# Optimization experiments

Hardware: AMD Instinct MI355X
Metric: run time of the kernel (lower is better)

## Reference

```python
import jax, jax.numpy as jnp
import numpy as np

B, T, D = 8, 1024, 768
N_HEAD = 12
HEAD_DIM = D // N_HEAD


def setup_inputs() -> dict:
    key = jax.random.key(0)
    k1, k2, k3, k4, k5 = jax.random.split(key, 5)
    x = jax.random.normal(k1, (B, T, D), dtype=jnp.float32)
    # c_attn: Linear(D, 3D); c_proj: Linear(D, D). Stored as (in, out) for x @ W.
    s_attn = 1.0 / np.sqrt(D)
    W_attn = jax.random.uniform(k2, (D, 3 * D), dtype=jnp.float32, minval=-s_attn, maxval=s_attn)
    b_attn = jax.random.uniform(k3, (3 * D,), dtype=jnp.float32, minval=-s_attn, maxval=s_attn)
    W_proj = jax.random.uniform(k4, (D, D), dtype=jnp.float32, minval=-s_attn, maxval=s_attn)
    b_proj = jax.random.uniform(k5, (D,), dtype=jnp.float32, minval=-s_attn, maxval=s_attn)
    return {"x": x, "W_attn": W_attn, "b_attn": b_attn, "W_proj": W_proj, "b_proj": b_proj}


def reference(x, W_attn, b_attn, W_proj, b_proj):
    Bs, Ts, Ds = x.shape
    qkv = x @ W_attn + b_attn  # [B, T, 3D]
    Q, K, V = jnp.split(qkv, 3, axis=2)
    # [B, H, T, hd]
    Q = Q.reshape(Bs, Ts, N_HEAD, HEAD_DIM).transpose(0, 2, 1, 3)
    K = K.reshape(Bs, Ts, N_HEAD, HEAD_DIM).transpose(0, 2, 1, 3)
    V = V.reshape(Bs, Ts, N_HEAD, HEAD_DIM).transpose(0, 2, 1, 3)
    scale = HEAD_DIM ** (-0.5)
    scores = jnp.einsum('bhqd,bhkd->bhqk', Q, K) * scale  # [B, H, T, T]
    causal = jnp.tril(jnp.ones((Ts, Ts), dtype=bool))
    scores = jnp.where(causal[None, None, :, :], scores, -jnp.inf)
    probs = jax.nn.softmax(scores, axis=-1)
    attn = jnp.einsum('bhqk,bhkd->bhqd', probs, V)  # [B, H, T, hd]
    attn = attn.transpose(0, 2, 1, 3).reshape(Bs, Ts, Ds)
    return attn @ W_proj + b_proj
```

## Files before the change

### kernel.cpp

```cpp
#include <hip/hip_runtime.h>
#include <hip/hip_bf16.h>

#define B_ 8
#define T_ 1024
#define D_ 768
#define NH 12
#define HD 64

typedef __bf16 bf16x8 __attribute__((ext_vector_type(8)));
typedef __bf16 bf16x4 __attribute__((ext_vector_type(4)));
typedef float f32x4 __attribute__((ext_vector_type(4)));
typedef short s16x4 __attribute__((ext_vector_type(4)));

__device__ __forceinline__ float fast_exp2(float x) {
  return __builtin_amdgcn_exp2f(x);
}

__device__ __forceinline__ f32x4 mfma32(bf16x8 a, bf16x8 b, f32x4 c) {
  return __builtin_amdgcn_mfma_f32_16x16x32_bf16(a, b, c, 0, 0, 0);
}

__device__ __forceinline__ f32x4 mfma16(bf16x4 a, bf16x4 b, f32x4 c) {
  union U { bf16x4 h; s16x4 s; };
  U ua; ua.h = a;
  U ub; ub.h = b;
  return __builtin_amdgcn_mfma_f32_16x16x16bf16_1k(ua.s, ub.s, c, 0, 0, 0);
}

__device__ __forceinline__ void gload_lds16(const void* g, void* l) {
  __builtin_amdgcn_global_load_lds((const __attribute__((address_space(1))) unsigned int*)g,
                                   (__attribute__((address_space(3))) unsigned int*)l, 16, 0, 0);
}

__global__ void prep_kernel(const float* __restrict__ x, __bf16* __restrict__ xb,
                            const float* __restrict__ W_attn, __bf16* __restrict__ WaT,
                            const float* __restrict__ W_proj, __bf16* __restrict__ WpT) {
  int bid = blockIdx.x;
  int tid = threadIdx.x;
  if (bid < 3072) {
    int i = bid * 256 + tid;
    const float4* xf = (const float4*)x;
    float4 a = xf[i * 2], b = xf[i * 2 + 1];
    bf16x8 v;
    v[0] = (__bf16)a.x; v[1] = (__bf16)a.y; v[2] = (__bf16)a.z; v[3] = (__bf16)a.w;
    v[4] = (__bf16)b.x; v[5] = (__bf16)b.y; v[6] = (__bf16)b.z; v[7] = (__bf16)b.w;
    *(bf16x8*)&xb[(size_t)i * 8] = v;
    return;
  }
  __shared__ float tile[32][33];
  const float* W;
  __bf16* WT;
  int K = 768, N, n0, k0;
  if (bid < 4800) {
    int i = bid - 3072;
    W = W_attn; WT = WaT; N = 2304;
    n0 = (i % 72) * 32; k0 = (i / 72) * 32;
  } else {
    int i = bid - 4800;
    W = W_proj; WT = WpT; N = 768;
    n0 = (i % 24) * 32; k0 = (i / 24) * 32;
  }
  int col = tid & 31, r0 = tid >> 5;
#pragma unroll
  for (int p = 0; p < 4; p++) {
    int r = r0 + p * 8;
    tile[r][col] = W[(size_t)(k0 + r) * N + n0 + col];
  }
  __syncthreads();
#pragma unroll
  for (int p = 0; p < 4; p++) {
    int r = r0 + p * 8;
    WT[(size_t)(n0 + r) * K + k0 + col] = (__bf16)tile[col][r];
  }
}

__global__ __launch_bounds__(256) void gemm_qkv(const __bf16* __restrict__ A,
                                                const __bf16* __restrict__ BT,
                                                const float* __restrict__ bias,
                                                __bf16* __restrict__ Cout,
                                                __bf16* __restrict__ VT,
                                                int M, int N, int K, int nbx) {
  __shared__ __align__(16) __bf16 Asm[2][128 * 64];
  __shared__ __align__(16) __bf16 Bsm[2][64 * 64];
  int tid = threadIdx.x;
  int wave = tid >> 6, lane = tid & 63, g = lane >> 4, l15 = lane & 15;

  int wg = blockIdx.x;
  int cpx = gridDim.x >> 3;
  int wg2 = (wg & 7) * cpx + (wg >> 3);
  int bx = wg2 % nbx, by = wg2 / nbx;
  int m0 = by * 128, n0 = bx * 64;

  int srow = tid >> 3;
  int cc = (tid & 7) ^ ((tid >> 3) & 7);
  const __bf16* Ag = A + (size_t)(m0 + srow) * K + cc * 8;
  const __bf16* Bg = BT + (size_t)(n0 + srow) * K + cc * 8;

  auto stage = [&](int kt, int bf) {
#pragma unroll
    for (int i = 0; i < 4; i++)
      gload_lds16(Ag + (size_t)(i * 32) * K + kt * 64, &Asm[bf][wave * 512 + i * 2048]);
#pragma unroll
    for (int i = 0; i < 2; i++)
      gload_lds16(Bg + (size_t)(i * 32) * K + kt * 64, &Bsm[bf][wave * 512 + i * 2048]);
  };

  f32x4 zz = {0.0f, 0.0f, 0.0f, 0.0f};
  f32x4 acc[2][4];
#pragma unroll
  for (int m = 0; m < 2; m++)
#pragma unroll
    for (int n = 0; n < 4; n++) acc[m][n] = zz;

  int nk = K >> 6;
  int swr = l15 & 7;

  stage(0, 0);
  __syncthreads();

  int cur = 0;
  for (int kt = 0; kt < nk; kt++) {
    if (kt + 1 < nk) stage(kt + 1, cur ^ 1);
#pragma unroll
    for (int ks = 0; ks < 2; ks++) {
      bf16x8 af[2], bfr[4];
#pragma unroll
      for (int m = 0; m < 2; m++) {
        int row = wave * 32 + m * 16 + l15;
        af[m] = *(const bf16x8*)&Asm[cur][row * 64 + ((ks * 4 + g) ^ swr) * 8];
      }
#pragma unroll
      for (int n = 0; n < 4; n++) {
        int row = n * 16 + l15;
        bfr[n] = *(const bf16x8*)&Bsm[cur][row * 64 + ((ks * 4 + g) ^ swr) * 8];
      }
#pragma unroll
      for (int m = 0; m < 2; m++)
#pragma unroll
        for (int n = 0; n < 4; n++)
          acc[m][n] = __builtin_amdgcn_mfma_f32_16x16x32_bf16(af[m], bfr[n], acc[m][n], 0, 0, 0);
    }
    __syncthreads();
    cur ^= 1;
  }
#pragma unroll
  for (int n = 0; n < 4; n++) {
    int gcol = n0 + n * 16 + l15;
    float bv = bias[gcol];
#pragma unroll
    for (int m = 0; m < 2; m++) {
      int grow0 = m0 + wave * 32 + m * 16 + g * 4;
      float v0 = acc[m][n][0] + bv, v1 = acc[m][n][1] + bv;
      float v2 = acc[m][n][2] + bv, v3 = acc[m][n][3] + bv;
      if (gcol < 2 * D_) {
        Cout[(size_t)(grow0 + 0) * N + gcol] = (__bf16)v0;
        Cout[(size_t)(grow0 + 1) * N + gcol] = (__bf16)v1;
        Cout[(size_t)(grow0 + 2) * N + gcol] = (__bf16)v2;
        Cout[(size_t)(grow0 + 3) * N + gcol] = (__bf16)v3;
      } else {
        int hh = (gcol - 2 * D_) >> 6, dd = (gcol - 2 * D_) & 63;
        int bb = grow0 >> 10, tt = grow0 & 1023;
        bf16x4 sv = {(__bf16)v0, (__bf16)v1, (__bf16)v2, (__bf16)v3};
        *(bf16x4*)&VT[((size_t)(bb * NH + hh) * HD + dd) * T_ + tt] = sv;
      }
    }
  }
}

__global__ __launch_bounds__(256) void gemm_proj(const __bf16* __restrict__ A,
                                                 const __bf16* __restrict__ BT,
                                                 const float* __restrict__ bias,
                                                 float* __restrict__ Cout,
                                                 int M, int N, int K, int nbx) {
  __shared__ __align__(16) __bf16 Asm[2][128 * 64];
  __shared__ __align__(16) __bf16 Bsm[2][64 * 64];
  int tid = threadIdx.x;
  int wave = tid >> 6, lane = tid & 63, g = lane >> 4, l15 = lane & 15;

  int wg = blockIdx.x;
  int cpx = gridDim.x >> 3;
  int wg2 = (wg & 7) * cpx + (wg >> 3);
  int bx = wg2 % nbx, by = wg2 / nbx;
  int m0 = by * 128, n0 = bx * 64;

  int srow = tid >> 3;
  int cc = (tid & 7) ^ ((tid >> 3) & 7);
  const __bf16* Ag = A + (size_t)(m0 + srow) * K + cc * 8;
  const __bf16* Bg = BT + (size_t)(n0 + srow) * K + cc * 8;

  auto stage = [&](int kt, int bf) {
#pragma unroll
    for (int i = 0; i < 4; i++)
      gload_lds16(Ag + (size_t)(i * 32) * K + kt * 64, &Asm[bf][wave * 512 + i * 2048]);
#pragma unroll
    for (int i = 0; i < 2; i++)
      gload_lds16(Bg + (size_t)(i * 32) * K + kt * 64, &Bsm[bf][wave * 512 + i * 2048]);
  };

  f32x4 zz = {0.0f, 0.0f, 0.0f, 0.0f};
  f32x4 acc[2][4];
#pragma unroll
  for (int m = 0; m < 2; m++)
#pragma unroll
    for (int n = 0; n < 4; n++) acc[m][n] = zz;

  int nk = K >> 6;
  int swr = l15 & 7;

  stage(0, 0);
  __syncthreads();

  int cur = 0;
  for (int kt = 0; kt < nk; kt++) {
    if (kt + 1 < nk) stage(kt + 1, cur ^ 1);
#pragma unroll
    for (int ks = 0; ks < 2; ks++) {
      bf16x8 af[2], bfr[4];
#pragma unroll
      for (int m = 0; m < 2; m++) {
        int row = wave * 32 + m * 16 + l15;
        af[m] = *(const bf16x8*)&Asm[cur][row * 64 + ((ks * 4 + g) ^ swr) * 8];
      }
#pragma unroll
      for (int n = 0; n < 4; n++) {
        int row = n * 16 + l15;
        bfr[n] = *(const bf16x8*)&Bsm[cur][row * 64 + ((ks * 4 + g) ^ swr) * 8];
      }
#pragma unroll
      for (int m = 0; m < 2; m++)
#pragma unroll
        for (int n = 0; n < 4; n++)
          acc[m][n] = __builtin_amdgcn_mfma_f32_16x16x32_bf16(af[m], bfr[n], acc[m][n], 0, 0, 0);
    }
    __syncthreads();
    cur ^= 1;
  }
#pragma unroll
  for (int n = 0; n < 4; n++) {
    int gcol = n0 + n * 16 + l15;
    float bv = bias[gcol];
#pragma unroll
    for (int m = 0; m < 2; m++) {
      int grow0 = m0 + wave * 32 + m * 16 + g * 4;
#pragma unroll
      for (int r = 0; r < 4; r++)
        Cout[(size_t)(grow0 + r) * N + gcol] = acc[m][n][r] + bv;
    }
  }
}

#define SCL 0.1803368801111204f

__global__ __launch_bounds__(256, 4) void attn_kernel(const __bf16* __restrict__ qkv,
                                                      const __bf16* __restrict__ VT,
                                                      __bf16* __restrict__ attn_out) {
  __shared__ __align__(16) __bf16 sm[2][2][4096];
  int tid = threadIdx.x;
  int wave = tid >> 6, lane = tid & 63, g = lane >> 4, l15 = lane & 15;
  int bh = blockIdx.x;
  int b = bh / NH, h = bh % NH;
  int qb = 15 - blockIdx.y;
  int q0w = qb * 64 + wave * 16;
  int nkt = qb + 1;
  int s0 = (bh + qb) % nkt;

  int kr = tid >> 3, cc = (tid & 7) ^ ((tid >> 3) & 7);
  const __bf16* Kst = qkv + (size_t)(b * T_ + kr) * (3 * D_) + D_ + h * HD + cc * 8;
  const __bf16* Vst = VT + ((size_t)bh * HD + kr) * T_ + cc * 8;
  __bf16* ldsK0 = &sm[0][0][wave * 512];
  __bf16* ldsV0 = &sm[0][1][wave * 512];
  __bf16* ldsK1 = &sm[1][0][wave * 512];
  __bf16* ldsV1 = &sm[1][1][wave * 512];

  auto stage = [&](int t, int bf) {
    size_t ko = (size_t)(t * 64) * (3 * D_);
    int vo = t * 64;
    __bf16* lk = bf ? ldsK1 : ldsK0;
    __bf16* lv = bf ? ldsV1 : ldsV0;
    gload_lds16(Kst + ko, lk);
    gload_lds16(Kst + ko + (size_t)32 * (3 * D_), lk + 2048);
    gload_lds16(Vst + vo, lv);
    gload_lds16(Vst + vo + 32 * T_, lv + 2048);
  };

  const __bf16* Qp = qkv + (size_t)(b * T_ + q0w + l15) * (3 * D_) + h * HD;
  bf16x8 qlo = *(const bf16x8*)(Qp + g * 8);
  bf16x8 qhi = *(const bf16x8*)(Qp + 32 + g * 8);

  f32x4 zz = {0.0f, 0.0f, 0.0f, 0.0f};
  f32x4 o0 = zz, o1 = zz, o2 = zz, o3 = zz;
  float m = -1e30f, l = 0.0f;
  int sw = l15 & 7;
  int clo = (g ^ sw) * 8;
  int chi = ((4 + g) ^ sw) * 8;

  stage(s0, 0);
  __syncthreads();

  int cur = 0;
  for (int i = 0; i < nkt; i++) {
    int kt = s0 + i;
    if (kt >= nkt) kt -= nkt;
    if (i + 1 < nkt) stage(kt + 1 == nkt ? 0 : kt + 1, cur ^ 1);

    const __bf16* Kb = &sm[cur][0][0];
    f32x4 s[4];
    __builtin_amdgcn_s_setprio(1);
#pragma unroll
    for (int kg = 0; kg < 4; kg++) {
      int rb = (kg * 16 + l15) * 64;
      bf16x8 kf = *(const bf16x8*)(Kb + rb + clo);
      bf16x8 kh = *(const bf16x8*)(Kb + rb + chi);
      s[kg] = mfma32(kf, qlo, zz);
      s[kg] = mfma32(kh, qhi, s[kg]);
    }
    __builtin_amdgcn_s_setprio(0);

    float v[16];
#pragma unroll
    for (int kg = 0; kg < 4; kg++)
#pragma unroll
      for (int r = 0; r < 4; r++) v[kg * 4 + r] = s[kg][r] * SCL;
    if (kt == qb) {
      int thr = wave * 16 + l15;
#pragma unroll
      for (int kg = 0; kg < 4; kg++)
#pragma unroll
        for (int r = 0; r < 4; r++)
          if (kg * 16 + g * 4 + r > thr) v[kg * 4 + r] = -1e30f;
    }
    float m0a = fmaxf(fmaxf(v[0], v[1]), fmaxf(v[2], v[3]));
    float m1a = fmaxf(fmaxf(v[4], v[5]), fmaxf(v[6], v[7]));
    float m2a = fmaxf(fmaxf(v[8], v[9]), fmaxf(v[10], v[11]));
    float m3a = fmaxf(fmaxf(v[12], v[13]), fmaxf(v[14], v[15]));
    float mx = fmaxf(fmaxf(m0a, m1a), fmaxf(m2a, m3a));
    mx = fmaxf(mx, __shfl_xor(mx, 16));
    mx = fmaxf(mx, __shfl_xor(mx, 32));
    if (!__all(mx <= m + 8.0f)) {
      float mnew = fmaxf(m, mx);
      float corr = fast_exp2(m - mnew);
      o0 *= corr; o1 *= corr; o2 *= corr; o3 *= corr;
      l *= corr;
      m = mnew;
    }
    float p[16], sum = 0.0f;
#pragma unroll
    for (int i2 = 0; i2 < 16; i2++) { p[i2] = fast_exp2(v[i2] - m); sum += p[i2]; }
    sum += __shfl_xor(sum, 16);
    sum += __shfl_xor(sum, 32);
    l += sum;
    bf16x4 pk[4];
#pragma unroll
    for (int kg = 0; kg < 4; kg++) {
      pk[kg][0] = (__bf16)p[kg * 4 + 0];
      pk[kg][1] = (__bf16)p[kg * 4 + 1];
      pk[kg][2] = (__bf16)p[kg * 4 + 2];
      pk[kg][3] = (__bf16)p[kg * 4 + 3];
    }

    const __bf16* Vb = &sm[cur][1][0];
    int vhalf = (g & 1) * 4;
    int vc = g >> 1;
    __builtin_amdgcn_s_setprio(1);
#pragma unroll
    for (int dq = 0; dq < 4; dq++) {
      int drow = (dq * 16 + l15) * 64;
#pragma unroll
      for (int ks = 0; ks < 4; ks++) {
        bf16x4 vf = *(const bf16x4*)(Vb + drow + ((ks * 2 + vc) ^ sw) * 8 + vhalf);
        f32x4* op = (dq == 0) ? &o0 : (dq == 1) ? &o1 : (dq == 2) ? &o2 : &o3;
        *op = mfma16(vf, pk[ks], *op);
      }
    }
    __builtin_amdgcn_s_setprio(0);

    __syncthreads();
    cur ^= 1;
  }

  float invl = 1.0f / l;
  __bf16* outp = attn_out + (size_t)(b * T_ + q0w + l15) * D_ + h * HD + g * 4;
  bf16x4 t0 = {(__bf16)(o0[0] * invl), (__bf16)(o0[1] * invl), (__bf16)(o0[2] * invl), (__bf16)(o0[3] * invl)};
  bf16x4 t1 = {(__bf16)(o1[0] * invl), (__bf16)(o1[1] * invl), (__bf16)(o1[2] * invl), (__bf16)(o1[3] * invl)};
  bf16x4 t2 = {(__bf16)(o2[0] * invl), (__bf16)(o2[1] * invl), (__bf16)(o2[2] * invl), (__bf16)(o2[3] * invl)};
  bf16x4 t3 = {(__bf16)(o3[0] * invl), (__bf16)(o3[1] * invl), (__bf16)(o3[2] * invl), (__bf16)(o3[3] * invl)};
  *(bf16x4*)(outp) = t0;
  *(bf16x4*)(outp + 16) = t1;
  *(bf16x4*)(outp + 32) = t2;
  *(bf16x4*)(outp + 48) = t3;
}

extern "C" void kernel_launch(void* const* d_in, const int* in_sizes, int n_in,
                              void* d_out, int out_size, void* d_ws, size_t ws_size,
                              hipStream_t stream) {
  (void)in_sizes; (void)n_in; (void)out_size; (void)ws_size;
  const float* x = (const float*)d_in[0];
  const float* W_attn = (const float*)d_in[1];
  const float* b_attn = (const float*)d_in[2];
  const float* W_proj = (const float*)d_in[3];
  const float* b_proj = (const float*)d_in[4];

  char* ws = (char*)d_ws;
  __bf16* xb  = (__bf16*)(ws + 0);
  __bf16* WaT = (__bf16*)(ws + 12582912);
  __bf16* WpT = (__bf16*)(ws + 16121856);
  __bf16* qkv = (__bf16*)(ws + 17301504);
  __bf16* VTb = (__bf16*)(ws + 55050240);
  __bf16* att = (__bf16*)(ws + 67633152);

  prep_kernel<<<dim3(5376), 256, 0, stream>>>(x, xb, W_attn, WaT, W_proj, WpT);
  gemm_qkv<<<dim3(2304), 256, 0, stream>>>(xb, WaT, b_attn, qkv, VTb, 8192, 2304, 768, 36);
  attn_kernel<<<dim3(96, 16), 256, 0, stream>>>(qkv, VTb, att);
  gemm_proj<<<dim3(768), 256, 0, stream>>>(att, WpT, b_proj, (float*)d_out, 8192, 768, 768, 12);
}
```

Before: 105.5 us.

## Fuse fp32-to-bf16 conversion of x into QKV GEMM A-tile loading

Drops the separate pass that converted x to bf16 in the prep kernel. The QKV GEMM now reads fp32 x straight into registers, converts it to bf16 and writes it into the swizzled LDS tile, while B still uses direct global-to-LDS loads. This removes a full read and write of the activation tensor and shrinks the prep launch. In exchange, every column tile block re-reads fp32 A, doubling A bytes fetched, and A staging now goes through registers, which raises register pressure and adds VALU conversion work inside the main loop.

```diff
diff --git a/kernel.cpp b/kernel.cpp
--- a/kernel.cpp
+++ b/kernel.cpp
@@ -32,31 +32,19 @@
                                    (__attribute__((address_space(3))) unsigned int*)l, 16, 0, 0);
 }
 
-__global__ void prep_kernel(const float* __restrict__ x, __bf16* __restrict__ xb,
-                            const float* __restrict__ W_attn, __bf16* __restrict__ WaT,
+__global__ void prep_kernel(const float* __restrict__ W_attn, __bf16* __restrict__ WaT,
                             const float* __restrict__ W_proj, __bf16* __restrict__ WpT) {
   int bid = blockIdx.x;
   int tid = threadIdx.x;
-  if (bid < 3072) {
-    int i = bid * 256 + tid;
-    const float4* xf = (const float4*)x;
-    float4 a = xf[i * 2], b = xf[i * 2 + 1];
-    bf16x8 v;
-    v[0] = (__bf16)a.x; v[1] = (__bf16)a.y; v[2] = (__bf16)a.z; v[3] = (__bf16)a.w;
-    v[4] = (__bf16)b.x; v[5] = (__bf16)b.y; v[6] = (__bf16)b.z; v[7] = (__bf16)b.w;
-    *(bf16x8*)&xb[(size_t)i * 8] = v;
-    return;
-  }
   __shared__ float tile[32][33];
   const float* W;
   __bf16* WT;
   int K = 768, N, n0, k0;
-  if (bid < 4800) {
-    int i = bid - 3072;
+  if (bid < 1728) {
     W = W_attn; WT = WaT; N = 2304;
-    n0 = (i % 72) * 32; k0 = (i / 72) * 32;
+    n0 = (bid % 72) * 32; k0 = (bid / 72) * 32;
   } else {
-    int i = bid - 4800;
+    int i = bid - 1728;
     W = W_proj; WT = WpT; N = 768;
     n0 = (i % 24) * 32; k0 = (i / 24) * 32;
   }
@@ -74,7 +62,7 @@
   }
 }
 
-__global__ __launch_bounds__(256) void gemm_qkv(const __bf16* __restrict__ A,
+__global__ __launch_bounds__(256) void gemm_qkv(const float* __restrict__ X,
                                                 const __bf16* __restrict__ BT,
                                                 const float* __restrict__ bias,
                                                 __bf16* __restrict__ Cout,
@@ -93,18 +81,36 @@
 
   int srow = tid >> 3;
   int cc = (tid & 7) ^ ((tid >> 3) & 7);
-  const __bf16* Ag = A + (size_t)(m0 + srow) * K + cc * 8;
+  const float* Ag = X + (size_t)(m0 + srow) * K + cc * 8;
   const __bf16* Bg = BT + (size_t)(n0 + srow) * K + cc * 8;
 
-  auto stage = [&](int kt, int bf) {
-#pragma unroll
-    for (int i = 0; i < 4; i++)
-      gload_lds16(Ag + (size_t)(i * 32) * K + kt * 64, &Asm[bf][wave * 512 + i * 2048]);
+  auto stageB = [&](int kt, int bf) {
 #pragma unroll
     for (int i = 0; i < 2; i++)
       gload_lds16(Bg + (size_t)(i * 32) * K + kt * 64, &Bsm[bf][wave * 512 + i * 2048]);
   };
 
+  float4 ar0[4], ar1[4];
+  auto loadA = [&](int kt) {
+#pragma unroll
+    for (int i = 0; i < 4; i++) {
+      const float4* p = (const float4*)(Ag + (size_t)(i * 32) * K + kt * 64);
+      ar0[i] = p[0];
+      ar1[i] = p[1];
+    }
+  };
+  auto writeA = [&](int bf) {
+#pragma unroll
+    for (int i = 0; i < 4; i++) {
+      bf16x8 v;
+      v[0] = (__bf16)ar0[i].x; v[1] = (__bf16)ar0[i].y;
+      v[2] = (__bf16)ar0[i].z; v[3] = (__bf16)ar0[i].w;
+      v[4] = (__bf16)ar1[i].x; v[5] = (__bf16)ar1[i].y;
+      v[6] = (__bf16)ar1[i].z; v[7] = (__bf16)ar1[i].w;
+      *(bf16x8*)&Asm[bf][i * 2048 + tid * 8] = v;
+    }
+  };
+
   f32x4 zz = {0.0f, 0.0f, 0.0f, 0.0f};
   f32x4 acc[2][4];
 #pragma unroll
@@ -115,12 +121,17 @@
   int nk = K >> 6;
   int swr = l15 & 7;
 
-  stage(0, 0);
+  loadA(0);
+  stageB(0, 0);
+  writeA(0);
   __syncthreads();
 
   int cur = 0;
   for (int kt = 0; kt < nk; kt++) {
-    if (kt + 1 < nk) stage(kt + 1, cur ^ 1);
+    if (kt + 1 < nk) {
+      stageB(kt + 1, cur ^ 1);
+      loadA(kt + 1);
+    }
 #pragma unroll
     for (int ks = 0; ks < 2; ks++) {
       bf16x8 af[2], bfr[4];
@@ -140,6 +151,7 @@
         for (int n = 0; n < 4; n++)
           acc[m][n] = __builtin_amdgcn_mfma_f32_16x16x32_bf16(af[m], bfr[n], acc[m][n], 0, 0, 0);
     }
+    if (kt + 1 < nk) writeA(cur ^ 1);
     __syncthreads();
     cur ^= 1;
   }
@@ -401,15 +413,14 @@
   const float* b_proj = (const float*)d_in[4];
 
   char* ws = (char*)d_ws;
-  __bf16* xb  = (__bf16*)(ws + 0);
   __bf16* WaT = (__bf16*)(ws + 12582912);
   __bf16* WpT = (__bf16*)(ws + 16121856);
   __bf16* qkv = (__bf16*)(ws + 17301504);
   __bf16* VTb = (__bf16*)(ws + 55050240);
   __bf16* att = (__bf16*)(ws + 67633152);
 
-  prep_kernel<<<dim3(5376), 256, 0, stream>>>(x, xb, W_attn, WaT, W_proj, WpT);
-  gemm_qkv<<<dim3(2304), 256, 0, stream>>>(xb, WaT, b_attn, qkv, VTb, 8192, 2304, 768, 36);
+  prep_kernel<<<dim3(2304), 256, 0, stream>>>(W_attn, WaT, W_proj, WpT);
+  gemm_qkv<<<dim3(2304), 256, 0, stream>>>(x, WaT, b_attn, qkv, VTb, 8192, 2304, 768, 36);
   attn_kernel<<<dim3(96, 16), 256, 0, stream>>>(qkv, VTb, att);
   gemm_proj<<<dim3(768), 256, 0, stream>>>(att, WpT, b_proj, (float*)d_out, 8192, 768, 768, 12);
 }
```

Result: slower. 120.3 us (+13.9%).
